# Kernel optimization log

Hardware: AMD Instinct MI355X
Metric: run time of the kernel (lower is better)

The kernel has to match this reference:

```python
import jax, jax.numpy as jnp
import numpy as np

T = 4            # timesteps (init arg T)
K = 8            # num_thresholds
B = 64           # batch per timestep (x.shape[0] == T*B)


def setup_inputs() -> dict:
    key = jax.random.key(0)
    kx, = jax.random.split(key, 1)
    x = jax.random.normal(kx, (T * B, 128, 32, 32), dtype=jnp.float32)
    thresh = jnp.asarray(1.0, dtype=jnp.float32)  # scalar learnable threshold
    return {"x": x, "thresh": thresh}


def reference(x, thresh):
    # thre_shaped: thresh / 2**k, shaped [K, 1,1,1,1] to broadcast over mem[None] = [1,B,C,H,W]
    thre = (thresh / (2.0 ** jnp.arange(K, dtype=x.dtype))).reshape((K,) + (1,) * x.ndim)
    thr75 = thre * 0.75

    xt = x.reshape((T, x.shape[0] // T) + x.shape[1:])  # expand: [T, B, C, H, W]

    def step(mem, xc):
        mem = mem + xc
        # which thresholds the membrane exceeds (thresholds are decreasing in k)
        pos = (mem[None] >= thr75).astype(x.dtype)           # [K, B, C, H, W]
        pos_true = pos.at[1:].add(-pos[:-1])                 # first (largest) crossed threshold only
        spike = jnp.sum(thre * pos_true, axis=0)             # [B, C, H, W]
        return mem - spike, spike

    mem0 = jnp.zeros_like(xt[0])
    _, spikes = jax.lax.scan(step, mem0, xt)                 # spikes: [T, B, C, H, W]
    return spikes.reshape(x.shape)                            # merge: [T*B, C, H, W]
```

## Files before the change

### kernel.cpp

```cpp
#include <hip/hip_runtime.h>


constexpr int T_STEPS = 4;
constexpr int BLOCK   = 1024;
constexpr int NXCD    = 8;

typedef float v4f __attribute__((ext_vector_type(4)));

__device__ __forceinline__ float spike_of(float mem, int b75_0, int b75_7, int bth0) {
    int u = __float_as_int(mem);
    int d = (int)((unsigned)b75_0 - (unsigned)u);
    int k = (int)((unsigned)d + 0x7fffffu) >> 23;
    k = k > 0 ? k : 0;
    int sb = bth0 - (k << 23);
    return (u >= b75_7) ? __int_as_float(sb) : 0.0f;
}

__global__ __launch_bounds__(BLOCK) void snn_mth_kernel(
    const float* __restrict__ x,
    const float* __restrict__ p_thresh,
    float* __restrict__ out,
    int s4)
{
    const float thresh = *p_thresh;
    const int bth0  = __float_as_int(thresh);
    const int b75_0 = __float_as_int(0.75f * thresh);
    const int b75_7 = b75_0 - 7 * 0x800000;

    const v4f* __restrict__ xv = reinterpret_cast<const v4f*>(x);
    v4f* __restrict__ ov = reinterpret_cast<v4f*>(out);

    const int seg_cols   = s4 / (NXCD * BLOCK) * BLOCK;
    const int seg_blocks = seg_cols / BLOCK;
    const int main_blocks = seg_blocks * NXCD;

    const int b = blockIdx.x;
    size_t j;
    if (b < main_blocks) {
        const int xcd  = b % NXCD;
        const int slot = b / NXCD;
        j = (size_t)xcd * seg_cols + (size_t)slot * BLOCK + threadIdx.x;
    } else {
        j = (size_t)NXCD * seg_cols + (size_t)(b - main_blocks) * BLOCK + threadIdx.x;
        if (j >= (size_t)s4) return;
    }

    const size_t n = (size_t)s4;

    v4f xc[T_STEPS];
#pragma unroll
    for (int t = 0; t < T_STEPS; ++t)
        xc[t] = xv[(size_t)t * n + j];

    v4f sp[T_STEPS];
#pragma unroll
    for (int e = 0; e < 4; ++e) {
        float mem = xc[0][e];
        float s0 = spike_of(mem, b75_0, b75_7, bth0);
        sp[0][e] = s0;
        mem = mem - s0 + xc[1][e];
        float s1 = spike_of(mem, b75_0, b75_7, bth0);
        sp[1][e] = s1;
        mem = mem - s1 + xc[2][e];
        float s2 = spike_of(mem, b75_0, b75_7, bth0);
        sp[2][e] = s2;
        mem = mem - s2 + xc[3][e];
        sp[3][e] = spike_of(mem, b75_0, b75_7, bth0);
    }

#pragma unroll
    for (int t = 0; t < T_STEPS; ++t)
        __builtin_nontemporal_store(sp[t], &ov[(size_t)t * n + j]);
}

extern "C" void kernel_launch(void* const* d_in, const int* in_sizes, int n_in,
                              void* d_out, int out_size, void* d_ws, size_t ws_size,
                              hipStream_t stream) {
    const float* x = (const float*)d_in[0];
    const float* p_thresh = (const float*)d_in[1];
    float* out = (float*)d_out;

    const int total = in_sizes[0];
    const int S = total / T_STEPS;
    const int s4 = S >> 2;

    const int grid = (s4 + BLOCK - 1) / BLOCK;
    snn_mth_kernel<<<grid, BLOCK, 0, stream>>>(x, p_thresh, out, s4);
}
```

Before: 242.1 us.

## Stage timestep tiles through LDS with rotated per-wave column offsets

Main blocks now load the four timestep slices into shared memory, with each timestep's column index rotated by a per-timestep offset. Different waves therefore hit different timestep streams at the same moment, which is meant to spread DRAM channel and bank traffic. Outputs are written back through LDS with the same rotation. This adds 64KB of LDS per block, three barriers and extra LDS traffic, which may reduce occupancy for a purely bandwidth-bound kernel.

```diff
diff --git a/kernel.cpp b/kernel.cpp
--- a/kernel.cpp
+++ b/kernel.cpp
@@ -3,6 +3,7 @@
 
 constexpr int T_STEPS = 4;
 constexpr int BLOCK   = 1024;
+constexpr int ROT     = 256;
 constexpr int NXCD    = 8;
 
 typedef float v4f __attribute__((ext_vector_type(4)));
@@ -30,47 +31,85 @@
     const v4f* __restrict__ xv = reinterpret_cast<const v4f*>(x);
     v4f* __restrict__ ov = reinterpret_cast<v4f*>(out);
 
+    __shared__ v4f lds[T_STEPS][BLOCK];
+
     const int seg_cols   = s4 / (NXCD * BLOCK) * BLOCK;
     const int seg_blocks = seg_cols / BLOCK;
     const int main_blocks = seg_blocks * NXCD;
 
-    const int b = blockIdx.x;
-    size_t j;
+    const int b   = blockIdx.x;
+    const int tid = threadIdx.x;
+    const size_t n = (size_t)s4;
+
     if (b < main_blocks) {
         const int xcd  = b % NXCD;
         const int slot = b / NXCD;
-        j = (size_t)xcd * seg_cols + (size_t)slot * BLOCK + threadIdx.x;
-    } else {
-        j = (size_t)NXCD * seg_cols + (size_t)(b - main_blocks) * BLOCK + threadIdx.x;
-        if (j >= (size_t)s4) return;
-    }
-
-    const size_t n = (size_t)s4;
-
-    v4f xc[T_STEPS];
-#pragma unroll
-    for (int t = 0; t < T_STEPS; ++t)
-        xc[t] = xv[(size_t)t * n + j];
-
-    v4f sp[T_STEPS];
-#pragma unroll
-    for (int e = 0; e < 4; ++e) {
-        float mem = xc[0][e];
-        float s0 = spike_of(mem, b75_0, b75_7, bth0);
-        sp[0][e] = s0;
-        mem = mem - s0 + xc[1][e];
-        float s1 = spike_of(mem, b75_0, b75_7, bth0);
-        sp[1][e] = s1;
-        mem = mem - s1 + xc[2][e];
-        float s2 = spike_of(mem, b75_0, b75_7, bth0);
-        sp[2][e] = s2;
-        mem = mem - s2 + xc[3][e];
-        sp[3][e] = spike_of(mem, b75_0, b75_7, bth0);
-    }
+        const size_t col0 = (size_t)xcd * seg_cols + (size_t)slot * BLOCK;
 
 #pragma unroll
-    for (int t = 0; t < T_STEPS; ++t)
-        __builtin_nontemporal_store(sp[t], &ov[(size_t)t * n + j]);
+        for (int t = 0; t < T_STEPS; ++t) {
+            const int cw = (tid + t * ROT) & (BLOCK - 1);
+            lds[t][cw] = xv[(size_t)t * n + col0 + cw];
+        }
+        __syncthreads();
+
+        v4f xc[T_STEPS];
+#pragma unroll
+        for (int t = 0; t < T_STEPS; ++t)
+            xc[t] = lds[t][tid];
+
+        v4f sp[T_STEPS];
+#pragma unroll
+        for (int e = 0; e < 4; ++e) {
+            float mem = xc[0][e];
+            float s0 = spike_of(mem, b75_0, b75_7, bth0);
+            sp[0][e] = s0;
+            mem = mem - s0 + xc[1][e];
+            float s1 = spike_of(mem, b75_0, b75_7, bth0);
+            sp[1][e] = s1;
+            mem = mem - s1 + xc[2][e];
+            float s2 = spike_of(mem, b75_0, b75_7, bth0);
+            sp[2][e] = s2;
+            mem = mem - s2 + xc[3][e];
+            sp[3][e] = spike_of(mem, b75_0, b75_7, bth0);
+        }
+
+        __syncthreads();
+#pragma unroll
+        for (int t = 0; t < T_STEPS; ++t)
+            lds[t][tid] = sp[t];
+        __syncthreads();
+#pragma unroll
+        for (int t = 0; t < T_STEPS; ++t) {
+            const int cw = (tid + t * ROT) & (BLOCK - 1);
+            __builtin_nontemporal_store(lds[t][cw], &ov[(size_t)t * n + col0 + cw]);
+        }
+    } else {
+        const size_t j = (size_t)NXCD * seg_cols + (size_t)(b - main_blocks) * BLOCK + tid;
+        if (j >= n) return;
+        v4f xc[T_STEPS];
+#pragma unroll
+        for (int t = 0; t < T_STEPS; ++t)
+            xc[t] = xv[(size_t)t * n + j];
+        v4f sp[T_STEPS];
+#pragma unroll
+        for (int e = 0; e < 4; ++e) {
+            float mem = xc[0][e];
+            float s0 = spike_of(mem, b75_0, b75_7, bth0);
+            sp[0][e] = s0;
+            mem = mem - s0 + xc[1][e];
+            float s1 = spike_of(mem, b75_0, b75_7, bth0);
+            sp[1][e] = s1;
+            mem = mem - s1 + xc[2][e];
+            float s2 = spike_of(mem, b75_0, b75_7, bth0);
+            sp[2][e] = s2;
+            mem = mem - s2 + xc[3][e];
+            sp[3][e] = spike_of(mem, b75_0, b75_7, bth0);
+        }
+#pragma unroll
+        for (int t = 0; t < T_STEPS; ++t)
+            __builtin_nontemporal_store(sp[t], &ov[(size_t)t * n + j]);
+    }
 }
 
 extern "C" void kernel_launch(void* const* d_in, const int* in_sizes, int n_in,
```

New measurement: 235.6 us. 1.03x faster.
